# Optimization experiments

Measured on AMD Instinct MI355X. Metric: run time of the kernel, lower is better.

## Reference

```python
import jax, jax.numpy as jnp
import numpy as np

B, S, D = 2, 2048, 1024
H = 16
DK = D // H


def setup_inputs() -> dict:
    key = jax.random.key(0)
    ks = jax.random.split(key, 5)
    std = np.sqrt(2.0 / (D + D))
    x = jax.random.normal(ks[0], (B, S, D), dtype=jnp.float32)
    wq = jax.random.normal(ks[1], (D, D), dtype=jnp.float32) * std
    wk = jax.random.normal(ks[2], (D, D), dtype=jnp.float32) * std
    wv = jax.random.normal(ks[3], (D, D), dtype=jnp.float32) * std
    wo = jax.random.normal(ks[4], (D, D), dtype=jnp.float32) * std
    return {"x": x, "wq": wq, "wk": wk, "wv": wv, "wo": wo}


def reference(x, wq, wk, wv, wo):
    # Linear: y = x @ W.T  (weight stored as [d_out, d_in])
    q = jnp.einsum("bsd,ed->bse", x, wq)
    k = jnp.einsum("bsd,ed->bse", x, wk)
    v = jnp.einsum("bsd,ed->bse", x, wv)
    # split heads: [B, S, H*DK] -> [B, H, S, DK]
    q = q.reshape(B, S, H, DK).transpose(0, 2, 1, 3)
    k = k.reshape(B, S, H, DK).transpose(0, 2, 1, 3)
    v = v.reshape(B, S, H, DK).transpose(0, 2, 1, 3)
    scale = 1.0 / jnp.sqrt(jnp.asarray(DK, dtype=x.dtype))
    scores = jnp.einsum("bhqd,bhkd->bhqk", q, k) * scale  # [B,H,S,S]
    causal = jnp.tril(jnp.ones((S, S), dtype=bool))
    scores = jnp.where(causal, scores, -jnp.inf)
    attn = jax.nn.softmax(scores, axis=-1)
    out = jnp.einsum("bhqk,bhkd->bhqd", attn, v)  # [B,H,S,DK]
    out = out.transpose(0, 2, 1, 3).reshape(B, S, D)
    return jnp.einsum("bsd,ed->bse", out, wo)
```

## Files before the change

kernel.cpp:

```cpp
#include <hip/hip_runtime.h>
#include <hip/hip_bf16.h>
#include <cstdint>

#define B_ 2
#define S_ 2048
#define D_ 1024
#define H_ 16
#define DK_ 64

#define LOG2E_S 0.18033688f

typedef __attribute__((ext_vector_type(8))) short bf16x8;
typedef __attribute__((ext_vector_type(4))) float f32x4;

__device__ __forceinline__ unsigned short f2bf(float f) {
  unsigned u = __float_as_uint(f);
  u = (u + 0x7FFFu + ((u >> 16) & 1u)) >> 16;
  return (unsigned short)u;
}

__device__ __forceinline__ unsigned short f2bf_hw(float f) {
  __hip_bfloat16 h = __float2bfloat16(f);
  return *reinterpret_cast<unsigned short*>(&h);
}

typedef __attribute__((address_space(1))) void gv_t;
typedef __attribute__((address_space(3))) void lv_t;
__device__ __forceinline__ void gl16(const void* g, void* l) {
  __builtin_amdgcn_global_load_lds((gv_t*)g, (lv_t*)l, 16, 0, 0);
}

__device__ __forceinline__ void stage8w(const unsigned short* gbase, size_t ldg,
                                        unsigned short* lds, int wave, int lane) {
  const int lr = lane >> 3;
  const int col8 = (lane & 7) ^ lr;
  gl16(gbase + (size_t)(wave * 8 + lr) * ldg + col8 * 8, lds + wave * 512);
}

__device__ __forceinline__ bf16x8 rdswz(const unsigned short* lds, int row, int col) {
  return *(const bf16x8*)&lds[row * 64 + (col ^ ((row & 7) << 3))];
}

__global__ void cvt_all_kernel(const float* __restrict__ x,
                               const float* __restrict__ w0, const float* __restrict__ w1,
                               const float* __restrict__ w2, const float* __restrict__ w3,
                               unsigned short* __restrict__ xo,
                               unsigned short* __restrict__ o0, unsigned short* __restrict__ o1,
                               unsigned short* __restrict__ o2, unsigned short* __restrict__ o3) {
  const int mat = blockIdx.y;
  const float* in = (mat == 0) ? x : (mat == 1) ? w0 : (mat == 2) ? w1 : (mat == 3) ? w2 : w3;
  unsigned short* out = (mat == 0) ? xo : (mat == 1) ? o0 : (mat == 2) ? o1 : (mat == 3) ? o2 : o3;
  const int n4 = (mat == 0) ? (B_ * S_ * D_ / 4) : (D_ * D_ / 4);
  int i = blockIdx.x * blockDim.x + threadIdx.x;
  if (i >= n4) return;
  const float4 v = reinterpret_cast<const float4*>(in)[i];
  ushort4 o;
  o.x = f2bf(v.x); o.y = f2bf(v.y); o.z = f2bf(v.z); o.w = f2bf(v.w);
  reinterpret_cast<ushort4*>(out)[i] = o;
}

#define BM 128
#define BK 64

template <typename OutT, bool TV2, int BNv, bool SCALEQ>
__global__ __launch_bounds__(256) void gemm_bt(
    const unsigned short* __restrict__ A,
    const unsigned short* __restrict__ B0, const unsigned short* __restrict__ B1,
    const unsigned short* __restrict__ B2,
    OutT* __restrict__ C0, OutT* __restrict__ C1, OutT* __restrict__ C2,
    int M, int N, int K) {
  constexpr int NFRAG = BNv / 32;
  __shared__ unsigned short lA[BM * BK];
  __shared__ unsigned short lB[BNv * BK];
  const int tid = threadIdx.x;
  const int wave = tid >> 6, lane = tid & 63;
  const int l16 = lane & 15, lqq = lane >> 4;
  const int wr = wave >> 1, wc = wave & 1;
  const int lr = lane >> 3;
  const int col8 = ((lane & 7) ^ lr) * 8;

  const int tilesPerMat = N / BNv;
  const int bx = blockIdx.x;
  const int mat = bx / tilesPerMat;
  const int n0 = (bx % tilesPerMat) * BNv;
  const unsigned short* Bm = (mat == 0) ? B0 : (mat == 1) ? B1 : B2;
  OutT* C = (mat == 0) ? C0 : (mat == 1) ? C1 : C2;
  const int m0 = blockIdx.y * BM;

  f32x4 acc[4][NFRAG] = {};

  for (int k0 = 0; k0 < K; k0 += BK) {
    __syncthreads();
#pragma unroll
    for (int c = wave; c < 16; c += 4)
      gl16(A + (size_t)(m0 + c * 8 + lr) * K + k0 + col8, &lA[c * 512]);
#pragma unroll
    for (int c = wave; c < BNv / 8; c += 4)
      gl16(Bm + (size_t)(n0 + c * 8 + lr) * K + k0 + col8, &lB[c * 512]);
    __syncthreads();
#pragma unroll
    for (int kk = 0; kk < BK / 32; ++kk) {
      bf16x8 af[4], bfr[NFRAG];
#pragma unroll
      for (int m = 0; m < 4; ++m)
        af[m] = rdswz(lA, wr * 64 + m * 16 + l16, kk * 32 + lqq * 8);
#pragma unroll
      for (int n = 0; n < NFRAG; ++n)
        bfr[n] = rdswz(lB, wc * (BNv / 2) + n * 16 + l16, kk * 32 + lqq * 8);
      __builtin_amdgcn_s_setprio(1);
#pragma unroll
      for (int m = 0; m < 4; ++m)
#pragma unroll
        for (int n = 0; n < NFRAG; ++n)
          acc[m][n] = __builtin_amdgcn_mfma_f32_16x16x32_bf16(af[m], bfr[n], acc[m][n], 0, 0, 0);
      __builtin_amdgcn_s_setprio(0);
    }
  }

  if (TV2 && mat == 2) {
    unsigned short* Vt = (unsigned short*)C;
#pragma unroll
    for (int m = 0; m < 4; ++m)
#pragma unroll
      for (int n = 0; n < NFRAG; ++n) {
        int r0 = m0 + wr * 64 + m * 16 + lqq * 4;
        int cidx = n0 + wc * (BNv / 2) + n * 16 + l16;
        int bb = r0 >> 11, s = r0 & 2047;
        int h = cidx >> 6, dv = cidx & 63;
        ushort4 o;
        o.x = f2bf(acc[m][n][0]); o.y = f2bf(acc[m][n][1]);
        o.z = f2bf(acc[m][n][2]); o.w = f2bf(acc[m][n][3]);
        *(ushort4*)(Vt + ((size_t)((bb * H_ + h) * DK_ + dv)) * S_ + s) = o;
      }
  } else {
    const float cscale = (SCALEQ && mat == 0) ? LOG2E_S : 1.0f;
#pragma unroll
    for (int m = 0; m < 4; ++m)
#pragma unroll
      for (int n = 0; n < NFRAG; ++n)
#pragma unroll
        for (int j = 0; j < 4; ++j) {
          int r = m0 + wr * 64 + m * 16 + lqq * 4 + j;
          int cidx = n0 + wc * (BNv / 2) + n * 16 + l16;
          float v = acc[m][n][j] * cscale;
          if constexpr (sizeof(OutT) == 4) C[(size_t)r * N + cidx] = v;
          else C[(size_t)r * N + cidx] = f2bf(v);
        }
  }
}

__global__ __launch_bounds__(512) void attn_kernel(
    const unsigned short* __restrict__ Qg, const unsigned short* __restrict__ Kg,
    const unsigned short* __restrict__ Vtg, unsigned short* __restrict__ Og) {
  __shared__ unsigned short sK[2][64 * 64];
  __shared__ unsigned short sVt[2][64 * 64];
  __shared__ unsigned short sP[8][16 * 64];
  const int tid = threadIdx.x, wave = tid >> 6, lane = tid & 63;
  const int side = wave >> 2, wq = wave & 3;
  const int l16 = lane & 15, lq = lane >> 4;
  const int id = blockIdx.x;
  const int bh = (id & 7) * 4 + ((id >> 3) & 3);
  const int g = (id >> 5) & 7;
  const int i = (id < 256) ? (15 - g) : g;
  const int b = bh >> 4, h = bh & 15;
  const int qtA = 2 * i, qtB = 2 * i + 1;
  const int qt_s = side ? qtB : qtA;
  const int NT = i + 1;
  const size_t tokbase = (size_t)b * S_ * D_ + h * DK_;
  const unsigned short* VtB = Vtg + (size_t)(b * H_ + h) * DK_ * S_;
  unsigned short* sPw = sP[wave];

  const unsigned short* qrow = Qg + tokbase + (size_t)(qt_s * 64 + wq * 16 + l16) * D_;
  bf16x8 aq0 = *(const bf16x8*)(qrow + lq * 8);
  bf16x8 aq1 = *(const bf16x8*)(qrow + 32 + lq * 8);

  const float THR2 = 11.5416f;
  const short ONE_BF = 0x3F80;
  const bf16x8 vones = {ONE_BF, ONE_BF, ONE_BF, ONE_BF, ONE_BF, ONE_BF, ONE_BF, ONE_BF};
  float m_run[4] = {-1e30f, -1e30f, -1e30f, -1e30f};
  f32x4 sum_acc = {};
  f32x4 o_acc[4] = {};

#pragma unroll 1
  for (int kt = 0; kt < NT; ++kt) {
    __syncthreads();
    stage8w(Kg + tokbase + (size_t)(kt * 128) * D_, D_, sK[0], wave, lane);
    stage8w(Kg + tokbase + (size_t)(kt * 128 + 64) * D_, D_, sK[1], wave, lane);
    stage8w(VtB + kt * 128, S_, sVt[0], wave, lane);
    stage8w(VtB + kt * 128 + 64, S_, sVt[1], wave, lane);
    __syncthreads();

    const bool last = (kt == NT - 1);
    float p[8][4];

#pragma unroll
    for (int sub = 0; sub < 2; ++sub) {
      const bool skip = (sub == 1) && (side == 0) && last;
      if (!skip) {
        __builtin_amdgcn_s_setprio(1);
#pragma unroll
        for (int nb = 0; nb < 4; ++nb) {
          bf16x8 bk0 = rdswz(sK[sub], nb * 16 + l16, lq * 8);
          bf16x8 bk1 = rdswz(sK[sub], nb * 16 + l16, 32 + lq * 8);
          f32x4 a = {};
          a = __builtin_amdgcn_mfma_f32_16x16x32_bf16(aq0, bk0, a, 0, 0, 0);
          a = __builtin_amdgcn_mfma_f32_16x16x32_bf16(aq1, bk1, a, 0, 0, 0);
#pragma unroll
          for (int j = 0; j < 4; ++j) p[sub * 4 + nb][j] = a[j];
        }
        __builtin_amdgcn_s_setprio(0);
      } else {
#pragma unroll
        for (int nb = 0; nb < 4; ++nb)
#pragma unroll
          for (int j = 0; j < 4; ++j) p[sub * 4 + nb][j] = -1e30f;
      }
    }

    if (last) {
      if (side == 0) {
#pragma unroll
        for (int nb = 0; nb < 4; ++nb)
#pragma unroll
          for (int j = 0; j < 4; ++j) {
            int kidx = nb * 16 + l16;
            int qidx = wq * 16 + lq * 4 + j;
            if (kidx > qidx) p[nb][j] = -1e30f;
          }
      } else {
#pragma unroll
        for (int nb = 0; nb < 4; ++nb)
#pragma unroll
          for (int j = 0; j < 4; ++j) {
            int kidx = nb * 16 + l16;
            int qidx = wq * 16 + lq * 4 + j;
            if (kidx > qidx) p[4 + nb][j] = -1e30f;
          }
      }
    }

    float pmax[4];
    bool ok = true;
#pragma unroll
    for (int j = 0; j < 4; ++j) {
      float r = p[0][j];
#pragma unroll
      for (int nbb = 1; nbb < 8; ++nbb) r = fmaxf(r, p[nbb][j]);
      pmax[j] = r;
      ok = ok && (r <= m_run[j] + THR2);
    }
    if (!__all((int)ok)) {
#pragma unroll
      for (int j = 0; j < 4; ++j) {
        float r = pmax[j];
#pragma unroll
        for (int d = 1; d < 16; d <<= 1) r = fmaxf(r, __shfl_xor(r, d));
        float mn = fmaxf(m_run[j], r);
        float alpha = exp2f(m_run[j] - mn);
        m_run[j] = mn;
        sum_acc[j] *= alpha;
#pragma unroll
        for (int nb = 0; nb < 4; ++nb) o_acc[nb][j] *= alpha;
      }
    }
#pragma unroll
    for (int j = 0; j < 4; ++j)
#pragma unroll
      for (int nbb = 0; nbb < 8; ++nbb)
        p[nbb][j] = exp2f(p[nbb][j] - m_run[j]);

    __builtin_amdgcn_s_setprio(1);
#pragma unroll
    for (int sub = 0; sub < 2; ++sub) {
#pragma unroll
      for (int j = 0; j < 4; ++j) {
        const int rw = lq * 4 + j;
#pragma unroll
        for (int nb = 0; nb < 4; ++nb)
          sPw[rw * 64 + (((nb * 16 + l16) ^ ((rw & 7) << 3)))] = f2bf_hw(p[sub * 4 + nb][j]);
      }
#pragma unroll
      for (int kk = 0; kk < 2; ++kk) {
        bf16x8 ap = rdswz(sPw, l16, kk * 32 + lq * 8);
        sum_acc = __builtin_amdgcn_mfma_f32_16x16x32_bf16(ap, vones, sum_acc, 0, 0, 0);
#pragma unroll
        for (int nb = 0; nb < 4; ++nb) {
          bf16x8 bv = rdswz(sVt[sub], nb * 16 + l16, kk * 32 + lq * 8);
          o_acc[nb] = __builtin_amdgcn_mfma_f32_16x16x32_bf16(ap, bv, o_acc[nb], 0, 0, 0);
        }
      }
    }
    __builtin_amdgcn_s_setprio(0);
  }

#pragma unroll
  for (int j = 0; j < 4; ++j) {
    float inv = 1.f / sum_acc[j];
#pragma unroll
    for (int nb = 0; nb < 4; ++nb) {
      int r = qt_s * 64 + wq * 16 + lq * 4 + j;
      Og[tokbase + (size_t)r * D_ + nb * 16 + l16] = f2bf(o_acc[nb][j] * inv);
    }
  }
}

extern "C" void kernel_launch(void* const* d_in, const int* in_sizes, int n_in,
                              void* d_out, int out_size, void* d_ws, size_t ws_size,
                              hipStream_t stream) {
  const float* x = (const float*)d_in[0];
  const float* wq = (const float*)d_in[1];
  const float* wk = (const float*)d_in[2];
  const float* wv = (const float*)d_in[3];
  const float* wo = (const float*)d_in[4];
  float* out = (float*)d_out;

  char* ws = (char*)d_ws;
  const size_t MB = 1024 * 1024;
  unsigned short* xb  = (unsigned short*)(ws + 0);
  unsigned short* wqb = (unsigned short*)(ws + 8 * MB);
  unsigned short* wkb = (unsigned short*)(ws + 10 * MB);
  unsigned short* wvb = (unsigned short*)(ws + 12 * MB);
  unsigned short* wob = (unsigned short*)(ws + 14 * MB);
  unsigned short* Qb  = (unsigned short*)(ws + 16 * MB);
  unsigned short* Kb  = (unsigned short*)(ws + 24 * MB);
  unsigned short* Vtb = (unsigned short*)(ws + 32 * MB);
  unsigned short* AOb = (unsigned short*)(ws + 40 * MB);

  const int M = B_ * S_;
  const int N = D_, K = D_;

  cvt_all_kernel<<<dim3(B_ * S_ * D_ / 4 / 256, 5), 256, 0, stream>>>(
      x, wq, wk, wv, wo, xb, wqb, wkb, wvb, wob);

  gemm_bt<unsigned short, true, 128, true><<<dim3(3 * (N / 128), M / BM), 256, 0, stream>>>(
      xb, wqb, wkb, wvb, Qb, Kb, Vtb, M, N, K);

  attn_kernel<<<dim3(512), 512, 0, stream>>>(Qb, Kb, Vtb, AOb);

  gemm_bt<float, false, 64, false><<<dim3(N / 64, M / BM), 256, 0, stream>>>(
      AOb, wob, wob, wob, out, out, out, M, N, K);
}
```

Before: 112.3 us.

## Split attention blocks into separate 4-wave blocks per query tile

```diff
diff --git a/kernel.cpp b/kernel.cpp
--- a/kernel.cpp
+++ b/kernel.cpp
@@ -30,11 +30,12 @@
   __builtin_amdgcn_global_load_lds((gv_t*)g, (lv_t*)l, 16, 0, 0);
 }
 
-__device__ __forceinline__ void stage8w(const unsigned short* gbase, size_t ldg,
+__device__ __forceinline__ void stage4w(const unsigned short* gbase, size_t ldg,
                                         unsigned short* lds, int wave, int lane) {
   const int lr = lane >> 3;
   const int col8 = (lane & 7) ^ lr;
   gl16(gbase + (size_t)(wave * 8 + lr) * ldg + col8 * 8, lds + wave * 512);
+  gl16(gbase + (size_t)((wave + 4) * 8 + lr) * ldg + col8 * 8, lds + (wave + 4) * 512);
 }
 
 __device__ __forceinline__ bf16x8 rdswz(const unsigned short* lds, int row, int col) {
@@ -149,28 +150,29 @@
   }
 }
 
-__global__ __launch_bounds__(512) void attn_kernel(
+__global__ __launch_bounds__(256) void attn_kernel(
     const unsigned short* __restrict__ Qg, const unsigned short* __restrict__ Kg,
     const unsigned short* __restrict__ Vtg, unsigned short* __restrict__ Og) {
   __shared__ unsigned short sK[2][64 * 64];
   __shared__ unsigned short sVt[2][64 * 64];
-  __shared__ unsigned short sP[8][16 * 64];
+  __shared__ unsigned short sP[4][16 * 64];
   const int tid = threadIdx.x, wave = tid >> 6, lane = tid & 63;
-  const int side = wave >> 2, wq = wave & 3;
   const int l16 = lane & 15, lq = lane >> 4;
   const int id = blockIdx.x;
-  const int bh = (id & 7) * 4 + ((id >> 3) & 3);
-  const int g = (id >> 5) & 7;
-  const int i = (id < 256) ? (15 - g) : g;
+  const int q4 = id >> 8;
+  const int base = id & 255;
+  const int gp = base & 7;
+  const int bh = base >> 3;
+  const int ii = (q4 < 2) ? gp : (15 - gp);
+  const int side = q4 & 1;
+  const int qt = 2 * ii + side;
+  const int NT = ii + 1;
   const int b = bh >> 4, h = bh & 15;
-  const int qtA = 2 * i, qtB = 2 * i + 1;
-  const int qt_s = side ? qtB : qtA;
-  const int NT = i + 1;
   const size_t tokbase = (size_t)b * S_ * D_ + h * DK_;
   const unsigned short* VtB = Vtg + (size_t)(b * H_ + h) * DK_ * S_;
   unsigned short* sPw = sP[wave];
 
-  const unsigned short* qrow = Qg + tokbase + (size_t)(qt_s * 64 + wq * 16 + l16) * D_;
+  const unsigned short* qrow = Qg + tokbase + (size_t)(qt * 64 + wave * 16 + l16) * D_;
   bf16x8 aq0 = *(const bf16x8*)(qrow + lq * 8);
   bf16x8 aq1 = *(const bf16x8*)(qrow + 32 + lq * 8);
 
@@ -184,10 +186,10 @@
 #pragma unroll 1
   for (int kt = 0; kt < NT; ++kt) {
     __syncthreads();
-    stage8w(Kg + tokbase + (size_t)(kt * 128) * D_, D_, sK[0], wave, lane);
-    stage8w(Kg + tokbase + (size_t)(kt * 128 + 64) * D_, D_, sK[1], wave, lane);
-    stage8w(VtB + kt * 128, S_, sVt[0], wave, lane);
-    stage8w(VtB + kt * 128 + 64, S_, sVt[1], wave, lane);
+    stage4w(Kg + tokbase + (size_t)(kt * 128) * D_, D_, sK[0], wave, lane);
+    stage4w(Kg + tokbase + (size_t)(kt * 128 + 64) * D_, D_, sK[1], wave, lane);
+    stage4w(VtB + kt * 128, S_, sVt[0], wave, lane);
+    stage4w(VtB + kt * 128 + 64, S_, sVt[1], wave, lane);
     __syncthreads();
 
     const bool last = (kt == NT - 1);
@@ -224,7 +226,7 @@
 #pragma unroll
           for (int j = 0; j < 4; ++j) {
             int kidx = nb * 16 + l16;
-            int qidx = wq * 16 + lq * 4 + j;
+            int qidx = wave * 16 + lq * 4 + j;
             if (kidx > qidx) p[nb][j] = -1e30f;
           }
       } else {
@@ -233,7 +235,7 @@
 #pragma unroll
           for (int j = 0; j < 4; ++j) {
             int kidx = nb * 16 + l16;
-            int qidx = wq * 16 + lq * 4 + j;
+            int qidx = wave * 16 + lq * 4 + j;
             if (kidx > qidx) p[4 + nb][j] = -1e30f;
           }
       }
@@ -298,7 +300,7 @@
     float inv = 1.f / sum_acc[j];
 #pragma unroll
     for (int nb = 0; nb < 4; ++nb) {
-      int r = qt_s * 64 + wq * 16 + lq * 4 + j;
+      int r = qt * 64 + wave * 16 + lq * 4 + j;
       Og[tokbase + (size_t)r * D_ + nb * 16 + l16] = f2bf(o_acc[nb][j] * inv);
     }
   }
@@ -335,7 +337,7 @@
   gemm_bt<unsigned short, true, 128, true><<<dim3(3 * (N / 128), M / BM), 256, 0, stream>>>(
       xb, wqb, wkb, wvb, Qb, Kb, Vtb, M, N, K);
 
-  attn_kernel<<<dim3(512), 512, 0, stream>>>(Qb, Kb, Vtb, AOb);
+  attn_kernel<<<dim3(1024), 256, 0, stream>>>(Qb, Kb, Vtb, AOb);
 
   gemm_bt<float, false, 64, false><<<dim3(N / 64, M / BM), 256, 0, stream>>>(
       AOb, wob, wob, wob, out, out, out, M, N, K);
```

Result: slower. 123.3 us (+9.8%).
